# Kernel optimization log

Measured on AMD Instinct MI355X. Metric: run time of the kernel, lower is better.

## Reference

```python
import jax, jax.numpy as jnp
import numpy as np

NUM_HEADS = 16

def setup_inputs() -> dict:
    key = jax.random.key(0)
    k1, k2, k3 = jax.random.split(key, 3)
    B, N, C = 2, 2048, 256
    hidden = 4 * C  # 1024
    head_dim = hidden // NUM_HEADS  # 64
    array = jax.random.normal(k1, (B, N, C), dtype=jnp.float32)
    Wqkv = jax.random.normal(k2, (C, 3 * hidden), dtype=jnp.float32) * 0.02
    # Original code projects to q.shape[-1] == head_dim (quirk preserved)
    Wout = jax.random.normal(k3, (hidden, head_dim), dtype=jnp.float32) * 0.02
    return {"array": array, "Wqkv": Wqkv, "Wout": Wout}

def reference(array, Wqkv, Wout):
    B, N, C = array.shape
    H = NUM_HEADS
    qkv = array @ Wqkv                      # (B, N, 3*hidden)
    q, k, v = jnp.split(qkv, 3, axis=-1)    # each (B, N, hidden)
    def to_heads(a):
        return a.reshape(B, N, H, -1).transpose(0, 2, 1, 3)  # (B, H, N, d)
    q, k, v = map(to_heads, (q, k, v))
    d = q.shape[-1]
    scores = jnp.einsum('bhid,bhjd->bhij', q, k) / jnp.sqrt(jnp.float32(d))
    attn = jax.nn.softmax(scores, axis=-1)   # dropout is deterministic no-op
    out = jnp.einsum('bhij,bhjd->bhid', attn, v)
    out = out.transpose(0, 2, 1, 3).reshape(B, N, H * d)  # (B, N, hidden)
    return out @ Wout                        # (B, N, head_dim)
```

## Files before the change

### kernel.cpp

```cpp
#include <hip/hip_runtime.h>
#include <hip/hip_bf16.h>
#include <math.h>

typedef __attribute__((ext_vector_type(8))) short bf16x8;
typedef __attribute__((ext_vector_type(4))) float f32x4;
typedef __attribute__((ext_vector_type(4))) unsigned u32x4;
typedef __attribute__((ext_vector_type(2))) unsigned u32x2;

union bfpack { u32x4 u; bf16x8 h; };

__device__ inline unsigned bfraw(float f) {
    union { float f; unsigned u; } x; x.f = f;
    return x.u + 0x8000u;
}
__device__ inline short f2bf(float f) { return (short)(bfraw(f) >> 16); }
__device__ inline unsigned pkbf(float lo, float hi) {
    return __builtin_amdgcn_perm(bfraw(hi), bfraw(lo), 0x07060302);
}
__device__ inline float fast_exp2(float x) {
#if __has_builtin(__builtin_amdgcn_exp2f)
    return __builtin_amdgcn_exp2f(x);
#else
    return exp2f(x);
#endif
}
__device__ inline void gl_lds16(const short* g, short* l) {
    __builtin_amdgcn_global_load_lds(
        (const __attribute__((address_space(1))) unsigned*)g,
        (__attribute__((address_space(3))) unsigned*)l, 16, 0, 0);
}
#define SCQ 0.18033688011112042f

__global__ __launch_bounds__(256) void qkv_kernel(
        const float* __restrict__ A, const float* __restrict__ W,
        short* __restrict__ Qb, short* __restrict__ Kb, short* __restrict__ Vt) {
    __shared__ short As[128 * 40];
    __shared__ short Bs[128 * 40];
    int m0 = blockIdx.x * 128;
    int n0 = blockIdx.y * 128;
    int t = threadIdx.x;
    int wave = t >> 6, lane = t & 63;
    int quad = lane >> 4, l16 = lane & 15;
    f32x4 acc[2][8] = {};
    for (int k0 = 0; k0 < 256; k0 += 32) {
        __syncthreads();
        {
            int row = t >> 1, kh = (t & 1) * 16;
            const float* src = A + (size_t)(m0 + row) * 256 + k0 + kh;
            f32x4 a0 = ((const f32x4*)src)[0], a1 = ((const f32x4*)src)[1],
                  a2 = ((const f32x4*)src)[2], a3 = ((const f32x4*)src)[3];
            bfpack v0, v1;
            v0.u[0] = pkbf(a0[0], a0[1]); v0.u[1] = pkbf(a0[2], a0[3]);
            v0.u[2] = pkbf(a1[0], a1[1]); v0.u[3] = pkbf(a1[2], a1[3]);
            v1.u[0] = pkbf(a2[0], a2[1]); v1.u[1] = pkbf(a2[2], a2[3]);
            v1.u[2] = pkbf(a3[0], a3[1]); v1.u[3] = pkbf(a3[2], a3[3]);
            *(bf16x8*)&As[row * 40 + kh]     = v0.h;
            *(bf16x8*)&As[row * 40 + kh + 8] = v1.h;
        }
        {
            int n = t & 127, kh = (t >> 7) * 16;
            const float* src = W + (size_t)(k0 + kh) * 3072 + n0 + n;
#pragma unroll
            for (int cc = 0; cc < 2; ++cc) {
                int clog = (kh >> 3) + cc;
                int pos = clog ^ (n & 3);
                unsigned* dst = (unsigned*)&Bs[n * 40 + pos * 8];
#pragma unroll
                for (int jj = 0; jj < 4; ++jj) {
                    float w0 = src[(size_t)(cc * 8 + 2 * jj) * 3072];
                    float w1 = src[(size_t)(cc * 8 + 2 * jj + 1) * 3072];
                    dst[jj] = pkbf(w0, w1);
                }
            }
        }
        __syncthreads();
        bf16x8 af[2], bfr[8];
#pragma unroll
        for (int s = 0; s < 2; ++s)
            af[s] = *(const bf16x8*)&As[(wave * 32 + s * 16 + l16) * 40 + quad * 8];
#pragma unroll
        for (int c = 0; c < 8; ++c) {
            int n = c * 16 + l16;
            bfr[c] = *(const bf16x8*)&Bs[n * 40 + (quad ^ (n & 3)) * 8];
        }
#pragma unroll
        for (int s = 0; s < 2; ++s)
#pragma unroll
            for (int c = 0; c < 8; ++c)
                acc[s][c] = __builtin_amdgcn_mfma_f32_16x16x32_bf16(af[s], bfr[c],
                                                                    acc[s][c], 0, 0, 0);
    }
    int sel = n0 >> 10;
    int b = m0 >> 11;
    int nb = (m0 & 2047) + wave * 32;
#pragma unroll
    for (int s = 0; s < 2; ++s) {
#pragma unroll
        for (int c = 0; c < 8; ++c) {
            int gc = n0 + c * 16 + l16;
            int h = (gc >> 6) & 15, dim = gc & 63;
            int n_base = nb + s * 16 + quad * 4;
            if (sel == 2) {
                u32x2 pk;
                pk[0] = pkbf(acc[s][c][0], acc[s][c][1]);
                pk[1] = pkbf(acc[s][c][2], acc[s][c][3]);
                *(u32x2*)&Vt[(((size_t)(b * 16 + h) * 64 + dim) << 11) + n_base] = pk;
            } else {
                short* dst = (sel == 0) ? Qb : Kb;
                float sc = (sel == 0) ? SCQ : 1.0f;
#pragma unroll
                for (int r = 0; r < 4; ++r)
                    dst[(((size_t)(b * 16 + h) * 2048 + n_base + r) << 6) + dim] =
                        f2bf(acc[s][c][r] * sc);
            }
        }
    }
}

__global__ __launch_bounds__(256, 2) void attn_kernel(
        const short* __restrict__ Qb, const short* __restrict__ Kb,
        const short* __restrict__ Vt, short* __restrict__ AO) {
    __shared__ short KT[2][64 * 64];
    __shared__ short VT[2][64 * 64];
    int bh = blockIdx.y, qt = blockIdx.x;
    int t = threadIdx.x, wave = t >> 6, lane = t & 63;
    int quad = lane >> 4, l16 = lane & 15;
    const short* Qp = Qb + (size_t)bh * (2048 * 64);
    const short* Kp = Kb + (size_t)bh * (2048 * 64);
    const short* Vp = Vt + (size_t)bh * (64 * 2048);
    int q0 = qt * 128 + wave * 32;

    bf16x8 qf[2][2];
#pragma unroll
    for (int sq = 0; sq < 2; ++sq) {
        const short* qp = Qp + (size_t)(q0 + sq * 16 + l16) * 64 + quad * 8;
        qf[sq][0] = *(const bf16x8*)qp;
        qf[sq][1] = *(const bf16x8*)(qp + 32);
    }
    int r8 = lane >> 3, p8 = lane & 7;
    int kr0 = wave * 16 + r8, kr1 = kr0 + 8;
    int swz0 = (kr0 & 3) | (((kr0 >> 3) & 1) << 2);
    int swz1 = (kr1 & 3) | (((kr1 >> 3) & 1) << 2);
    const short* gk0 = Kp + kr0 * 64 + (p8 ^ swz0) * 8;
    const short* gk1 = Kp + kr1 * 64 + (p8 ^ swz1) * 8;
    const short* gv0 = Vp + kr0 * 2048 + (p8 ^ (kr0 & 7)) * 8;
    const short* gv1 = Vp + kr1 * 2048 + (p8 ^ (kr1 & 7)) * 8;
    int ldsk0 = wave * 1024, ldsk1 = wave * 1024 + 512;
    int swzk = (l16 & 3) | (((l16 >> 2) & 1) << 2);
    int krd = ((l16 >> 2) * 8 + (l16 & 3)) * 64;
    int koff0 = krd + ((quad ^ swzk) * 8);
    int koff1 = krd + (((quad + 4) ^ swzk) * 8);
    int voff0 = l16 * 64 + ((quad ^ (l16 & 7)) * 8);
    int voff1 = l16 * 64 + (((quad + 4) ^ (l16 & 7)) * 8);

    f32x4 o[2][4] = {};
    f32x4 ol[2] = {};
    bf16x8 ones = {(short)0x3F80, (short)0x3F80, (short)0x3F80, (short)0x3F80,
                   (short)0x3F80, (short)0x3F80, (short)0x3F80, (short)0x3F80};

    gl_lds16(gk0, &KT[0][ldsk0]);
    gl_lds16(gk1, &KT[0][ldsk1]);
    gl_lds16(gv0, &VT[0][ldsk0]);
    gl_lds16(gv1, &VT[0][ldsk1]);

    for (int kt = 0; kt < 32; ++kt) {
        __syncthreads();
        if (kt + 1 < 32) {
            int buf = (kt + 1) & 1;
            gl_lds16(gk0 + (size_t)(kt + 1) * 4096, &KT[buf][ldsk0]);
            gl_lds16(gk1 + (size_t)(kt + 1) * 4096, &KT[buf][ldsk1]);
            gl_lds16(gv0 + (kt + 1) * 64, &VT[buf][ldsk0]);
            gl_lds16(gv1 + (kt + 1) * 64, &VT[buf][ldsk1]);
        }
        const short* kb = &KT[kt & 1][0];
        const short* vb = &VT[kt & 1][0];
        bf16x8 kc[8], vc[8];
#pragma unroll
        for (int hh = 0; hh < 2; ++hh)
#pragma unroll
            for (int ab = 0; ab < 2; ++ab) {
                kc[(hh * 2 + ab) * 2 + 0] = *(const bf16x8*)&kb[koff0 + ab * 256 + hh * 2048];
                kc[(hh * 2 + ab) * 2 + 1] = *(const bf16x8*)&kb[koff1 + ab * 256 + hh * 2048];
            }
#pragma unroll
        for (int hh = 0; hh < 2; ++hh)
#pragma unroll
            for (int dt = 0; dt < 4; ++dt)
                vc[hh * 4 + dt] = *(const bf16x8*)&vb[(hh ? voff1 : voff0) + dt * 1024];

#pragma unroll
        for (int sq = 0; sq < 2; ++sq) {
            f32x4 s[4];
#pragma unroll
            for (int i = 0; i < 4; ++i) {
                f32x4 z = {};
                z = __builtin_amdgcn_mfma_f32_16x16x32_bf16(kc[2 * i], qf[sq][0], z, 0, 0, 0);
                z = __builtin_amdgcn_mfma_f32_16x16x32_bf16(kc[2 * i + 1], qf[sq][1], z, 0, 0, 0);
                s[i] = z;
            }
            bfpack pa0, pa1;
#pragma unroll
            for (int ab = 0; ab < 2; ++ab) {
                float p0 = fast_exp2(s[ab][0]),     p1 = fast_exp2(s[ab][1]);
                float p2 = fast_exp2(s[ab][2]),     p3 = fast_exp2(s[ab][3]);
                float q0e = fast_exp2(s[2 + ab][0]), q1e = fast_exp2(s[2 + ab][1]);
                float q2e = fast_exp2(s[2 + ab][2]), q3e = fast_exp2(s[2 + ab][3]);
                pa0.u[ab * 2 + 0] = pkbf(p0, p1);
                pa0.u[ab * 2 + 1] = pkbf(p2, p3);
                pa1.u[ab * 2 + 0] = pkbf(q0e, q1e);
                pa1.u[ab * 2 + 1] = pkbf(q2e, q3e);
            }
            ol[sq] = __builtin_amdgcn_mfma_f32_16x16x32_bf16(pa0.h, ones, ol[sq], 0, 0, 0);
            ol[sq] = __builtin_amdgcn_mfma_f32_16x16x32_bf16(pa1.h, ones, ol[sq], 0, 0, 0);
#pragma unroll
            for (int dt = 0; dt < 4; ++dt) {
                o[sq][dt] = __builtin_amdgcn_mfma_f32_16x16x32_bf16(pa0.h, vc[dt],
                                                                    o[sq][dt], 0, 0, 0);
                o[sq][dt] = __builtin_amdgcn_mfma_f32_16x16x32_bf16(pa1.h, vc[4 + dt],
                                                                    o[sq][dt], 0, 0, 0);
            }
        }
    }
#pragma unroll
    for (int sq = 0; sq < 2; ++sq) {
        f32x4 inv;
#pragma unroll
        for (int r = 0; r < 4; ++r) inv[r] = 1.0f / ol[sq][r];
#pragma unroll
        for (int dt = 0; dt < 4; ++dt)
#pragma unroll
            for (int r = 0; r < 4; ++r) {
                int qrow = q0 + sq * 16 + quad * 4 + r;
                AO[((size_t)bh * 2048 + qrow) * 64 + dt * 16 + l16] =
                    f2bf(o[sq][dt][r] * inv[r]);
            }
    }
}

__global__ __launch_bounds__(256) void out_kernel(
        const short* __restrict__ AO, const float* __restrict__ W,
        float* __restrict__ Out) {
    __shared__ short As[64 * 72];
    __shared__ short Bs[64 * 72];
    int m0 = blockIdx.x * 64;
    int t = threadIdx.x, wave = t >> 6, lane = t & 63;
    int quad = lane >> 4, l16 = lane & 15;
    int b = m0 >> 11;
    f32x4 acc[4] = {};
    for (int h = 0; h < 16; ++h) {
        __syncthreads();
        {
            int row = t >> 2, kh = (t & 3) * 16;
            const short* src = AO + ((size_t)(b * 16 + h) * 2048 + (m0 & 2047) + row) * 64 + kh;
            bf16x8 w0 = *(const bf16x8*)src;
            bf16x8 w1 = *(const bf16x8*)(src + 8);
            int c0 = (kh >> 3), c1 = c0 + 1;
            *(bf16x8*)&As[row * 72 + (c0 ^ (row & 7)) * 8] = w0;
            *(bf16x8*)&As[row * 72 + (c1 ^ (row & 7)) * 8] = w1;
        }
        {
            int n = t & 63, kh = (t >> 6) * 16;
            const float* src = W + (size_t)(h * 64 + kh) * 64 + n;
#pragma unroll
            for (int cc = 0; cc < 2; ++cc) {
                int clog = (kh >> 3) + cc;
                unsigned* dst = (unsigned*)&Bs[n * 72 + (clog ^ (n & 7)) * 8];
#pragma unroll
                for (int jj = 0; jj < 4; ++jj) {
                    float w0 = src[(size_t)(cc * 8 + 2 * jj) * 64];
                    float w1 = src[(size_t)(cc * 8 + 2 * jj + 1) * 64];
                    dst[jj] = pkbf(w0, w1);
                }
            }
        }
        __syncthreads();
        bf16x8 af[2], bfr[4][2];
        int arow = wave * 16 + l16;
#pragma unroll
        for (int kf = 0; kf < 2; ++kf)
            af[kf] = *(const bf16x8*)&As[arow * 72 + (((quad + 4 * kf) ^ (arow & 7)) * 8)];
#pragma unroll
        for (int c = 0; c < 4; ++c) {
            int n = c * 16 + l16;
#pragma unroll
            for (int kf = 0; kf < 2; ++kf)
                bfr[c][kf] = *(const bf16x8*)&Bs[n * 72 + (((quad + 4 * kf) ^ (n & 7)) * 8)];
        }
#pragma unroll
        for (int c = 0; c < 4; ++c) {
            acc[c] = __builtin_amdgcn_mfma_f32_16x16x32_bf16(af[0], bfr[c][0], acc[c], 0, 0, 0);
            acc[c] = __builtin_amdgcn_mfma_f32_16x16x32_bf16(af[1], bfr[c][1], acc[c], 0, 0, 0);
        }
    }
#pragma unroll
    for (int c = 0; c < 4; ++c)
#pragma unroll
        for (int r = 0; r < 4; ++r) {
            int gm = m0 + wave * 16 + quad * 4 + r;
            Out[((size_t)gm << 6) + c * 16 + l16] = acc[c][r];
        }
}

extern "C" void kernel_launch(void* const* d_in, const int* in_sizes, int n_in,
                              void* d_out, int out_size, void* d_ws, size_t ws_size,
                              hipStream_t stream) {
    const float* A    = (const float*)d_in[0];
    const float* Wqkv = (const float*)d_in[1];
    const float* Wout = (const float*)d_in[2];
    float* Out = (float*)d_out;

    short* ws = (short*)d_ws;
    short* Qb = ws;
    short* Kb = ws + 4194304;
    short* Vt = ws + 8388608;
    short* AO = ws + 12582912;

    hipLaunchKernelGGL(qkv_kernel, dim3(32, 24), dim3(256), 0, stream, A, Wqkv, Qb, Kb, Vt);
    hipLaunchKernelGGL(attn_kernel, dim3(16, 32), dim3(256), 0, stream, Qb, Kb, Vt, AO);
    hipLaunchKernelGGL(out_kernel, dim3(64), dim3(256), 0, stream, AO, Wout, Out);
}
```

Before: 145.3 us.

## Pre-transpose weights to bf16 and use direct global-to-LDS loads in GEMMs

Adds a transpose kernel that converts Wqkv and Wout to bf16 in N-major layout each call, so the QKV and output GEMMs can stream weight tiles with global_load_lds instead of strided fp32 loads plus packing. The QKV GEMM K-tile grows from 32 to 64 with an XOR-swizzled 64-wide LDS layout. Attention now writes its output as (B,N,H*D) so the output GEMM reads contiguous K rows. Two extra kernel launches and an extra weight pass are added in exchange for cheaper inner loops.

```diff
diff --git a/kernel.cpp b/kernel.cpp
--- a/kernel.cpp
+++ b/kernel.cpp
@@ -31,64 +31,102 @@
 }
 #define SCQ 0.18033688011112042f
 
+__global__ __launch_bounds__(256) void trans_kernel(
+        const float* __restrict__ src, short* __restrict__ dst, int R, int C) {
+    __shared__ float T[64][65];
+    int r0 = blockIdx.y * 64, c0 = blockIdx.x * 64;
+    int t = threadIdx.x;
+    {
+        int kr = t >> 2, ns = (t & 3) * 16;
+        const float* s = src + (size_t)(r0 + kr) * C + c0 + ns;
+#pragma unroll
+        for (int j = 0; j < 4; ++j) {
+            f32x4 v = *(const f32x4*)(s + j * 4);
+#pragma unroll
+            for (int e = 0; e < 4; ++e) T[kr][ns + j * 4 + e] = v[e];
+        }
+    }
+    __syncthreads();
+    {
+        int n = t >> 2, ks = (t & 3) * 16;
+        bfpack p0, p1;
+#pragma unroll
+        for (int j = 0; j < 4; ++j) {
+            float a = T[ks + 2 * j][n], b = T[ks + 2 * j + 1][n];
+            p0.u[j] = pkbf(a, b);
+        }
+#pragma unroll
+        for (int j = 0; j < 4; ++j) {
+            float a = T[ks + 8 + 2 * j][n], b = T[ks + 8 + 2 * j + 1][n];
+            p1.u[j] = pkbf(a, b);
+        }
+        short* d = dst + (size_t)(c0 + n) * R + r0 + ks;
+        *(bf16x8*)d = p0.h;
+        *(bf16x8*)(d + 8) = p1.h;
+    }
+}
+
 __global__ __launch_bounds__(256) void qkv_kernel(
-        const float* __restrict__ A, const float* __restrict__ W,
+        const float* __restrict__ A, const short* __restrict__ Wt,
         short* __restrict__ Qb, short* __restrict__ Kb, short* __restrict__ Vt) {
-    __shared__ short As[128 * 40];
-    __shared__ short Bs[128 * 40];
+    __shared__ short As[128 * 64];
+    __shared__ short Bs[128 * 64];
     int m0 = blockIdx.x * 128;
     int n0 = blockIdx.y * 128;
     int t = threadIdx.x;
     int wave = t >> 6, lane = t & 63;
     int quad = lane >> 4, l16 = lane & 15;
+    int r8 = lane >> 3, c8 = lane & 7;
     f32x4 acc[2][8] = {};
-    for (int k0 = 0; k0 < 256; k0 += 32) {
-        __syncthreads();
+    for (int it = 0; it < 4; ++it) {
+        int k0 = it * 64;
+        __syncthreads();
+#pragma unroll
+        for (int j = 0; j < 4; ++j) {
+            int row = wave * 32 + j * 8 + r8;
+            int clog = c8 ^ (row & 7);
+            gl_lds16(Wt + (size_t)(n0 + row) * 256 + k0 + clog * 8,
+                     &Bs[(wave * 32 + j * 8) * 64]);
+        }
         {
-            int row = t >> 1, kh = (t & 1) * 16;
-            const float* src = A + (size_t)(m0 + row) * 256 + k0 + kh;
-            f32x4 a0 = ((const f32x4*)src)[0], a1 = ((const f32x4*)src)[1],
-                  a2 = ((const f32x4*)src)[2], a3 = ((const f32x4*)src)[3];
-            bfpack v0, v1;
-            v0.u[0] = pkbf(a0[0], a0[1]); v0.u[1] = pkbf(a0[2], a0[3]);
-            v0.u[2] = pkbf(a1[0], a1[1]); v0.u[3] = pkbf(a1[2], a1[3]);
-            v1.u[0] = pkbf(a2[0], a2[1]); v1.u[1] = pkbf(a2[2], a2[3]);
-            v1.u[2] = pkbf(a3[0], a3[1]); v1.u[3] = pkbf(a3[2], a3[3]);
-            *(bf16x8*)&As[row * 40 + kh]     = v0.h;
-            *(bf16x8*)&As[row * 40 + kh + 8] = v1.h;
-        }
-        {
-            int n = t & 127, kh = (t >> 7) * 16;
-            const float* src = W + (size_t)(k0 + kh) * 3072 + n0 + n;
+            int row = t >> 1, half = t & 1;
+            const float* as = A + (size_t)(m0 + row) * 256 + k0 + half * 32;
 #pragma unroll
             for (int cc = 0; cc < 2; ++cc) {
-                int clog = (kh >> 3) + cc;
-                int pos = clog ^ (n & 3);
-                unsigned* dst = (unsigned*)&Bs[n * 40 + pos * 8];
-#pragma unroll
-                for (int jj = 0; jj < 4; ++jj) {
-                    float w0 = src[(size_t)(cc * 8 + 2 * jj) * 3072];
-                    float w1 = src[(size_t)(cc * 8 + 2 * jj + 1) * 3072];
-                    dst[jj] = pkbf(w0, w1);
-                }
-            }
-        }
-        __syncthreads();
-        bf16x8 af[2], bfr[8];
-#pragma unroll
-        for (int s = 0; s < 2; ++s)
-            af[s] = *(const bf16x8*)&As[(wave * 32 + s * 16 + l16) * 40 + quad * 8];
+                f32x4 a0 = ((const f32x4*)as)[cc * 4 + 0];
+                f32x4 a1 = ((const f32x4*)as)[cc * 4 + 1];
+                f32x4 a2 = ((const f32x4*)as)[cc * 4 + 2];
+                f32x4 a3 = ((const f32x4*)as)[cc * 4 + 3];
+                bfpack v0, v1;
+                v0.u[0] = pkbf(a0[0], a0[1]); v0.u[1] = pkbf(a0[2], a0[3]);
+                v0.u[2] = pkbf(a1[0], a1[1]); v0.u[3] = pkbf(a1[2], a1[3]);
+                v1.u[0] = pkbf(a2[0], a2[1]); v1.u[1] = pkbf(a2[2], a2[3]);
+                v1.u[2] = pkbf(a3[0], a3[1]); v1.u[3] = pkbf(a3[2], a3[3]);
+                int cl0 = half * 4 + cc * 2;
+                *(bf16x8*)&As[row * 64 + ((cl0    ) ^ (row & 7)) * 8] = v0.h;
+                *(bf16x8*)&As[row * 64 + ((cl0 + 1) ^ (row & 7)) * 8] = v1.h;
+            }
+        }
+        __syncthreads();
+        bf16x8 af[2][2];
+#pragma unroll
+        for (int s = 0; s < 2; ++s) {
+            int m = wave * 32 + s * 16 + l16;
+#pragma unroll
+            for (int kh = 0; kh < 2; ++kh)
+                af[s][kh] = *(const bf16x8*)&As[m * 64 + (((quad + 4 * kh)) ^ (m & 7)) * 8];
+        }
 #pragma unroll
         for (int c = 0; c < 8; ++c) {
             int n = c * 16 + l16;
-            bfr[c] = *(const bf16x8*)&Bs[n * 40 + (quad ^ (n & 3)) * 8];
-        }
-#pragma unroll
-        for (int s = 0; s < 2; ++s)
-#pragma unroll
-            for (int c = 0; c < 8; ++c)
-                acc[s][c] = __builtin_amdgcn_mfma_f32_16x16x32_bf16(af[s], bfr[c],
-                                                                    acc[s][c], 0, 0, 0);
+            bf16x8 b0 = *(const bf16x8*)&Bs[n * 64 + ((quad    ) ^ (n & 7)) * 8];
+            bf16x8 b1 = *(const bf16x8*)&Bs[n * 64 + ((quad + 4) ^ (n & 7)) * 8];
+#pragma unroll
+            for (int s = 0; s < 2; ++s) {
+                acc[s][c] = __builtin_amdgcn_mfma_f32_16x16x32_bf16(af[s][0], b0, acc[s][c], 0, 0, 0);
+                acc[s][c] = __builtin_amdgcn_mfma_f32_16x16x32_bf16(af[s][1], b1, acc[s][c], 0, 0, 0);
+            }
+        }
     }
     int sel = n0 >> 10;
     int b = m0 >> 11;
@@ -123,6 +161,7 @@
     __shared__ short KT[2][64 * 64];
     __shared__ short VT[2][64 * 64];
     int bh = blockIdx.y, qt = blockIdx.x;
+    int b = bh >> 4, h = bh & 15;
     int t = threadIdx.x, wave = t >> 6, lane = t & 63;
     int quad = lane >> 4, l16 = lane & 15;
     const short* Qp = Qb + (size_t)bh * (2048 * 64);
@@ -201,8 +240,8 @@
             bfpack pa0, pa1;
 #pragma unroll
             for (int ab = 0; ab < 2; ++ab) {
-                float p0 = fast_exp2(s[ab][0]),     p1 = fast_exp2(s[ab][1]);
-                float p2 = fast_exp2(s[ab][2]),     p3 = fast_exp2(s[ab][3]);
+                float p0 = fast_exp2(s[ab][0]),      p1 = fast_exp2(s[ab][1]);
+                float p2 = fast_exp2(s[ab][2]),      p3 = fast_exp2(s[ab][3]);
                 float q0e = fast_exp2(s[2 + ab][0]), q1e = fast_exp2(s[2 + ab][1]);
                 float q2e = fast_exp2(s[2 + ab][2]), q3e = fast_exp2(s[2 + ab][3]);
                 pa0.u[ab * 2 + 0] = pkbf(p0, p1);
@@ -231,65 +270,45 @@
 #pragma unroll
             for (int r = 0; r < 4; ++r) {
                 int qrow = q0 + sq * 16 + quad * 4 + r;
-                AO[((size_t)bh * 2048 + qrow) * 64 + dt * 16 + l16] =
+                AO[((size_t)(b * 2048 + qrow)) * 1024 + h * 64 + dt * 16 + l16] =
                     f2bf(o[sq][dt][r] * inv[r]);
             }
     }
 }
 
 __global__ __launch_bounds__(256) void out_kernel(
-        const short* __restrict__ AO, const float* __restrict__ W,
+        const short* __restrict__ AO, const short* __restrict__ Wo,
         float* __restrict__ Out) {
-    __shared__ short As[64 * 72];
-    __shared__ short Bs[64 * 72];
+    __shared__ short As[64 * 64];
+    __shared__ short Bs[64 * 64];
     int m0 = blockIdx.x * 64;
     int t = threadIdx.x, wave = t >> 6, lane = t & 63;
     int quad = lane >> 4, l16 = lane & 15;
-    int b = m0 >> 11;
+    int r8 = lane >> 3, c8 = lane & 7;
     f32x4 acc[4] = {};
-    for (int h = 0; h < 16; ++h) {
-        __syncthreads();
-        {
-            int row = t >> 2, kh = (t & 3) * 16;
-            const short* src = AO + ((size_t)(b * 16 + h) * 2048 + (m0 & 2047) + row) * 64 + kh;
-            bf16x8 w0 = *(const bf16x8*)src;
-            bf16x8 w1 = *(const bf16x8*)(src + 8);
-            int c0 = (kh >> 3), c1 = c0 + 1;
-            *(bf16x8*)&As[row * 72 + (c0 ^ (row & 7)) * 8] = w0;
-            *(bf16x8*)&As[row * 72 + (c1 ^ (row & 7)) * 8] = w1;
-        }
-        {
-            int n = t & 63, kh = (t >> 6) * 16;
-            const float* src = W + (size_t)(h * 64 + kh) * 64 + n;
-#pragma unroll
-            for (int cc = 0; cc < 2; ++cc) {
-                int clog = (kh >> 3) + cc;
-                unsigned* dst = (unsigned*)&Bs[n * 72 + (clog ^ (n & 7)) * 8];
-#pragma unroll
-                for (int jj = 0; jj < 4; ++jj) {
-                    float w0 = src[(size_t)(cc * 8 + 2 * jj) * 64];
-                    float w1 = src[(size_t)(cc * 8 + 2 * jj + 1) * 64];
-                    dst[jj] = pkbf(w0, w1);
-                }
-            }
-        }
-        __syncthreads();
-        bf16x8 af[2], bfr[4][2];
-        int arow = wave * 16 + l16;
-#pragma unroll
-        for (int kf = 0; kf < 2; ++kf)
-            af[kf] = *(const bf16x8*)&As[arow * 72 + (((quad + 4 * kf) ^ (arow & 7)) * 8)];
+    for (int it = 0; it < 16; ++it) {
+        int k0 = it * 64;
+        __syncthreads();
+#pragma unroll
+        for (int j = 0; j < 2; ++j) {
+            int row = wave * 16 + j * 8 + r8;
+            int clog = c8 ^ (row & 7);
+            gl_lds16(AO + (size_t)(m0 + row) * 1024 + k0 + clog * 8,
+                     &As[(wave * 16 + j * 8) * 64]);
+            gl_lds16(Wo + (size_t)row * 1024 + k0 + clog * 8,
+                     &Bs[(wave * 16 + j * 8) * 64]);
+        }
+        __syncthreads();
+        int m = wave * 16 + l16;
+        bf16x8 a0 = *(const bf16x8*)&As[m * 64 + ((quad    ) ^ (m & 7)) * 8];
+        bf16x8 a1 = *(const bf16x8*)&As[m * 64 + ((quad + 4) ^ (m & 7)) * 8];
 #pragma unroll
         for (int c = 0; c < 4; ++c) {
             int n = c * 16 + l16;
-#pragma unroll
-            for (int kf = 0; kf < 2; ++kf)
-                bfr[c][kf] = *(const bf16x8*)&Bs[n * 72 + (((quad + 4 * kf) ^ (n & 7)) * 8)];
-        }
-#pragma unroll
-        for (int c = 0; c < 4; ++c) {
-            acc[c] = __builtin_amdgcn_mfma_f32_16x16x32_bf16(af[0], bfr[c][0], acc[c], 0, 0, 0);
-            acc[c] = __builtin_amdgcn_mfma_f32_16x16x32_bf16(af[1], bfr[c][1], acc[c], 0, 0, 0);
+            bf16x8 b0 = *(const bf16x8*)&Bs[n * 64 + ((quad    ) ^ (n & 7)) * 8];
+            bf16x8 b1 = *(const bf16x8*)&Bs[n * 64 + ((quad + 4) ^ (n & 7)) * 8];
+            acc[c] = __builtin_amdgcn_mfma_f32_16x16x32_bf16(a0, b0, acc[c], 0, 0, 0);
+            acc[c] = __builtin_amdgcn_mfma_f32_16x16x32_bf16(a1, b1, acc[c], 0, 0, 0);
         }
     }
 #pragma unroll
@@ -310,12 +329,16 @@
     float* Out = (float*)d_out;
 
     short* ws = (short*)d_ws;
-    short* Qb = ws;
-    short* Kb = ws + 4194304;
-    short* Vt = ws + 8388608;
-    short* AO = ws + 12582912;
-
-    hipLaunchKernelGGL(qkv_kernel, dim3(32, 24), dim3(256), 0, stream, A, Wqkv, Qb, Kb, Vt);
+    short* Wq = ws;
+    short* Wo = ws + 786432;
+    short* Qb = ws + 851968;
+    short* Kb = ws + 5046272;
+    short* Vt = ws + 9240576;
+    short* AO = ws + 13434880;
+
+    hipLaunchKernelGGL(trans_kernel, dim3(48, 4), dim3(256), 0, stream, Wqkv, Wq, 256, 3072);
+    hipLaunchKernelGGL(trans_kernel, dim3(1, 16), dim3(256), 0, stream, Wout, Wo, 1024, 64);
+    hipLaunchKernelGGL(qkv_kernel, dim3(32, 24), dim3(256), 0, stream, A, Wq, Qb, Kb, Vt);
     hipLaunchKernelGGL(attn_kernel, dim3(16, 32), dim3(256), 0, stream, Qb, Kb, Vt, AO);
-    hipLaunchKernelGGL(out_kernel, dim3(64), dim3(256), 0, stream, AO, Wout, Out);
-}
+    hipLaunchKernelGGL(out_kernel, dim3(64), dim3(256), 0, stream, AO, Wo, Out);
+}
```

Result: faster. 138.4 us (-4.8%).
